# Optimization experiments

Measured on AMD Instinct MI355X. Metric: run time of the kernel, lower is better.

The kernel has to match this reference:

```python
import jax, jax.numpy as jnp
import numpy as np

B, S, D, H, DK, DV = 4, 1024, 1024, 16, 64, 64
NEG = jnp.float32(-1e10)


def setup_inputs() -> dict:
    key = jax.random.key(0)
    ks = jax.random.split(key, 9)
    q = jax.random.normal(ks[0], (B, S, D), dtype=jnp.float32)
    k = jax.random.normal(ks[1], (B, S, D), dtype=jnp.float32)
    v = jax.random.normal(ks[2], (B, S, D), dtype=jnp.float32)
    pad_mask_1 = jax.random.randint(ks[3], (B,), 1, S + 1, dtype=jnp.int32)
    pad_mask_2 = jax.random.randint(ks[4], (B,), 1, S + 1, dtype=jnp.int32)
    # Per-head projection weights stacked over heads (torch Linear, bias=False).
    sc = 1.0 / np.sqrt(D)
    Wq = jax.random.uniform(ks[5], (H, D, DK), jnp.float32, -sc, sc)
    Wk = jax.random.uniform(ks[6], (H, D, DK), jnp.float32, -sc, sc)
    Wv = jax.random.uniform(ks[7], (H, D, DV), jnp.float32, -sc, sc)
    Wo = jax.random.uniform(ks[8], (H * DV, D), jnp.float32, -sc, sc)
    return {"q": q, "k": k, "v": v, "pad_mask_1": pad_mask_1,
            "pad_mask_2": pad_mask_2, "Wq": Wq, "Wk": Wk, "Wv": Wv, "Wo": Wo}


def reference(q, k, v, pad_mask_1, pad_mask_2, Wq, Wk, Wv, Wo):
    Bq, Sq, _ = q.shape
    scale = jnp.sqrt(jnp.float32(Wq.shape[-1]))
    qh = jnp.einsum('bsd,hdk->bhsk', q, Wq)   # [B,H,S,DK]
    kh = jnp.einsum('bsd,hdk->bhsk', k, Wk)
    vh = jnp.einsum('bsd,hdv->bhsv', v, Wv)
    w = jnp.einsum('bhqk,bhtk->bhqt', qh, kh) / scale  # [B,H,S,S]
    idx = jnp.arange(Sq)
    # pad_mask_1: mask key columns >= length; pad_mask_2: mask query rows >= length
    key_dead = idx[None, :] >= pad_mask_1[:, None]      # [B,S]
    row_dead = idx[None, :] >= pad_mask_2[:, None]      # [B,S]
    w = jnp.where(key_dead[:, None, None, :], NEG, w)
    w = jnp.where(row_dead[:, None, :, None], NEG, w)
    # causal: w.tril() + (-1e10).triu(1) == keep lower triangle, NEG strictly above
    causal = idx[None, :] > idx[:, None]                # [S,S] strictly upper
    w = jnp.where(causal[None, None], NEG, w)
    a = jax.nn.softmax(w, axis=-1)
    o = jnp.einsum('bhqt,bhtv->bhqv', a, vh)            # [B,H,S,DV]
    o = o.transpose(0, 2, 1, 3).reshape(Bq, Sq, -1)     # concat heads (head-major)
    return o @ Wo
```

## Files before the change

kernel.cpp:

```cpp
#include <hip/hip_runtime.h>

#define B_ 4
#define S_ 1024
#define D_ 1024
#define H_ 16
#define BSD (B_*S_*D_)

typedef unsigned short ushort_t;
typedef __attribute__((ext_vector_type(8))) __bf16 bf16x8;
typedef __attribute__((ext_vector_type(4))) float f32x4;

__device__ __forceinline__ ushort_t f2bf(float f) {
  union { float f; unsigned int u; } x; x.f = f;
  unsigned int r = x.u + 0x7fffu + ((x.u >> 16) & 1u);
  return (ushort_t)(r >> 16);
}

__device__ __forceinline__ void gll16(const void* g, void* l) {
  __builtin_amdgcn_global_load_lds(
      (const __attribute__((address_space(1))) unsigned int*)g,
      (__attribute__((address_space(3))) unsigned int*)l, 16, 0, 0);
}

__global__ __launch_bounds__(256) void convert_qkv(
    const float* __restrict__ q, const float* __restrict__ k, const float* __restrict__ v,
    ushort_t* __restrict__ qb, ushort_t* __restrict__ kb, ushort_t* __restrict__ vb)
{
  int z = blockIdx.y;
  const float* src = (z == 0) ? q : (z == 1) ? k : v;
  ushort_t* dst = (z == 0) ? qb : (z == 1) ? kb : vb;
  int idx = (blockIdx.x * 256 + threadIdx.x) * 4;
  float4 f = *(const float4*)(src + idx);
  ushort4 r;
  r.x = f2bf(f.x); r.y = f2bf(f.y); r.z = f2bf(f.z); r.w = f2bf(f.w);
  *(ushort4*)(dst + idx) = r;
}

__global__ __launch_bounds__(256) void transpose_w(
    const float* __restrict__ Wq, const float* __restrict__ Wk,
    const float* __restrict__ Wv, const float* __restrict__ Wo,
    ushort_t* __restrict__ WqT, ushort_t* __restrict__ WkT,
    ushort_t* __restrict__ WvT, ushort_t* __restrict__ WoT)
{
  __shared__ float tile[64][65];
  int blk = blockIdx.x;
  const float* src; ushort_t* dst;
  size_t sbase, dbase; int ld_src, ld_dst, r0, c0;
  if (blk < 768) {
    int tz = blk / 256;
    int rem = blk % 256; int head = rem >> 4; int kt = rem & 15;
    src = (tz == 0) ? Wq : (tz == 1) ? Wk : Wv;
    dst = (tz == 0) ? WqT : (tz == 1) ? WkT : WvT;
    sbase = (size_t)head * 1024 * 64; dbase = (size_t)head * 64 * 1024;
    ld_src = 64; ld_dst = 1024; r0 = kt * 64; c0 = 0;
  } else {
    int idx = blk - 768; src = Wo; dst = WoT;
    sbase = 0; dbase = 0; ld_src = 1024; ld_dst = 1024;
    r0 = (idx >> 4) * 64; c0 = (idx & 15) * 64;
  }
  int tid = threadIdx.x; int col = tid & 63; int rbase = tid >> 6;
  #pragma unroll
  for (int j = 0; j < 16; ++j) {
    int row = j * 4 + rbase;
    tile[row][col] = src[sbase + (size_t)(r0 + row) * ld_src + c0 + col];
  }
  __syncthreads();
  #pragma unroll
  for (int j = 0; j < 16; ++j) {
    int orow = j * 4 + rbase;
    dst[dbase + (size_t)(c0 + orow) * ld_dst + r0 + col] = f2bf(tile[col][orow]);
  }
}

__device__ __forceinline__ void gemm_body(
    const ushort_t* __restrict__ A, const ushort_t* __restrict__ BT,
    ushort_t* __restrict__ Cb, float* __restrict__ Cf,
    int epi, int m0, int n0, int K)
{
  __shared__ __align__(16) ushort_t As[2][128 * 64];
  __shared__ __align__(16) ushort_t Bs[2][128 * 64];
  const int tid = threadIdx.x;
  const int wave = tid >> 6, lane = tid & 63;
  const int wm = wave >> 2, wn = wave & 3;

  f32x4 acc[4][2] = {};

  auto stage = [&](int buf, int k0) {
    #pragma unroll
    for (int i = 0; i < 2; ++i) {
      int off = ((i * 8 + wave) << 10) + lane * 16;
      int row = off >> 7;
      int cb = off & 127;
      int lcb = cb ^ ((row & 7) << 4);
      gll16(A + (size_t)(m0 + row) * K + k0 + (lcb >> 1), (char*)As[buf] + off);
      gll16(BT + (size_t)(n0 + row) * K + k0 + (lcb >> 1), (char*)Bs[buf] + off);
    }
  };

  auto compute = [&](int buf) {
    #pragma unroll
    for (int kk = 0; kk < 2; ++kk) {
      bf16x8 af[4], bfr[2];
      #pragma unroll
      for (int mf = 0; mf < 4; ++mf) {
        int row = wm * 64 + mf * 16 + (lane & 15);
        int cb = kk * 64 + ((lane >> 4) << 4);
        af[mf] = *(const bf16x8*)((const char*)As[buf] + (row << 7) + (cb ^ ((row & 7) << 4)));
      }
      #pragma unroll
      for (int nf = 0; nf < 2; ++nf) {
        int row = wn * 32 + nf * 16 + (lane & 15);
        int cb = kk * 64 + ((lane >> 4) << 4);
        bfr[nf] = *(const bf16x8*)((const char*)Bs[buf] + (row << 7) + (cb ^ ((row & 7) << 4)));
      }
      #pragma unroll
      for (int mf = 0; mf < 4; ++mf)
        #pragma unroll
        for (int nf = 0; nf < 2; ++nf)
          acc[mf][nf] = __builtin_amdgcn_mfma_f32_16x16x32_bf16(af[mf], bfr[nf], acc[mf][nf], 0, 0, 0);
    }
  };

  const int nt = K >> 6;
  stage(0, 0);
  __syncthreads();
  int cur = 0;
  for (int t = 0; t < nt - 1; ++t) {
    stage(cur ^ 1, (t + 1) << 6);
    compute(cur);
    __syncthreads();
    cur ^= 1;
  }
  compute(cur);

  #pragma unroll
  for (int mf = 0; mf < 4; ++mf) {
    #pragma unroll
    for (int nf = 0; nf < 2; ++nf) {
      #pragma unroll
      for (int r = 0; r < 4; ++r) {
        int m = m0 + wm * 64 + mf * 16 + ((lane >> 4) << 2) + r;
        int n = n0 + wn * 32 + nf * 16 + (lane & 15);
        float val = acc[mf][nf][r];
        if (epi == 0) {
          int b = m >> 10, s = m & 1023, h = n >> 6, dk = n & 63;
          Cb[((((size_t)(b * H_ + h)) << 10) + s) * 64 + dk] = f2bf(val);
        } else if (epi == 1) {
          int b = m >> 10, s = m & 1023, h = n >> 6, dv = n & 63;
          Cb[((((size_t)(b * H_ + h)) * 64 + dv) << 10) + s] = f2bf(val);
        } else {
          Cf[(size_t)m * 1024 + n] = val;
        }
      }
    }
  }
}

__global__ __launch_bounds__(512, 4) void proj_gemm(
    const ushort_t* qb, const ushort_t* kb, const ushort_t* vb,
    const ushort_t* WqT, const ushort_t* WkT, const ushort_t* WvT,
    ushort_t* qh, ushort_t* kh, ushort_t* vhT)
{
  int f = blockIdx.x;
  int xcd = f & 7;
  int slot = f >> 3;
  int g = xcd * 12 + (slot >> 3);
  int y = slot & 7;
  int z = g >> 5, x = g & 31;
  const ushort_t* A = (z == 0) ? qb : (z == 1) ? kb : vb;
  const ushort_t* BT = (z == 0) ? WqT : (z == 1) ? WkT : WvT;
  ushort_t* C = (z == 0) ? qh : (z == 1) ? kh : vhT;
  gemm_body(A, BT, C, nullptr, (z == 2) ? 1 : 0, x * 128, y * 128, 1024);
}

__global__ __launch_bounds__(512, 4) void out_gemm(
    const ushort_t* o, const ushort_t* WoT, float* out)
{
  int f = blockIdx.x;
  int xcd = f & 7;
  int slot = f >> 3;
  int x = xcd * 4 + (slot >> 3);
  int y = slot & 7;
  gemm_body(o, WoT, nullptr, out, 2, x * 128, y * 128, 1024);
}

__global__ __launch_bounds__(256) void meanv_kernel(
    const ushort_t* __restrict__ vhT, float* __restrict__ meanV)
{
  int row = blockIdx.x * 4 + (threadIdx.x >> 6);
  int lane = threadIdx.x & 63;
  const ushort_t* src = vhT + ((size_t)row << 10) + lane * 16;
  float s = 0.f;
  #pragma unroll
  for (int i = 0; i < 2; ++i) {
    bf16x8 v = *(const bf16x8*)(src + i * 8);
    #pragma unroll
    for (int j = 0; j < 8; ++j) s += (float)v[j];
  }
  #pragma unroll
  for (int mm = 1; mm < 64; mm <<= 1) s += __shfl_xor(s, mm);
  if (lane == 0) meanV[row] = s * (1.0f / 1024.0f);
}

__global__ __launch_bounds__(256) void attn_kernel(
    const ushort_t* __restrict__ qh, const ushort_t* __restrict__ kh,
    const ushort_t* __restrict__ vhT, const float* __restrict__ meanV,
    const int* __restrict__ pad1p, const int* __restrict__ pad2p,
    ushort_t* __restrict__ o)
{
  const int bh = blockIdx.x;
  const int b = bh >> 4, h = bh & 15;
  const int q0 = blockIdx.y << 6;
  const int pad1 = pad1p[b], pad2 = pad2p[b];
  const int tid = threadIdx.x, wave = tid >> 6, lane = tid & 63;

  if (q0 >= pad2) {
    int dv = tid & 63;
    int rw = tid >> 6;
    ushort_t mb = f2bf(meanV[(bh << 6) + dv]);
    for (int r = rw; r < 64; r += 4)
      o[(((size_t)((b << 10) + q0 + r)) << 10) + (h << 6) + dv] = mb;
    return;
  }

  __shared__ __align__(16) ushort_t Ks[64 * 64];
  __shared__ __align__(16) ushort_t Vs[64 * 64];
  __shared__ __align__(16) ushort_t Ps[4][16 * 64];

  const ushort_t* qbase = qh + ((size_t)bh << 16);
  const ushort_t* kbase = kh + ((size_t)bh << 16);
  const ushort_t* vbase = vhT + ((size_t)bh << 16);

  const int qrow = q0 + wave * 16 + (lane & 15);
  bf16x8 qf[2];
  qf[0] = *(const bf16x8*)(qbase + (size_t)qrow * 64 + ((lane >> 4) << 3));
  qf[1] = *(const bf16x8*)(qbase + (size_t)qrow * 64 + 32 + ((lane >> 4) << 3));

  f32x4 acc[4] = {};
  float mrow[4] = { -1e30f, -1e30f, -1e30f, -1e30f };
  float lrow[4] = { 0.f, 0.f, 0.f, 0.f };
  const int ribase = q0 + wave * 16 + ((lane >> 4) << 2);

  int t_hi = min(q0 + 63, min(pad2 - 1, pad1 - 1));
  int nb = (t_hi >> 6) + 1;

  for (int kb = 0; kb < nb; ++kb) {
    const int t0 = kb << 6;
    #pragma unroll
    for (int i = 0; i < 2; ++i) {
      int off = ((i * 4 + wave) << 10) + lane * 16;
      int row = off >> 7;
      int cb = off & 127;
      int lcb = cb ^ ((row & 7) << 4);
      gll16(kbase + (size_t)(t0 + row) * 64 + (lcb >> 1), (char*)Ks + off);
      gll16(vbase + ((size_t)row << 10) + t0 + (lcb >> 1), (char*)Vs + off);
    }
    __syncthreads();

    f32x4 sc[4];
    #pragma unroll
    for (int nf = 0; nf < 4; ++nf) {
      sc[nf] = (f32x4){0.f, 0.f, 0.f, 0.f};
      #pragma unroll
      for (int kk = 0; kk < 2; ++kk) {
        int trow = nf * 16 + (lane & 15);
        int cb = kk * 64 + ((lane >> 4) << 4);
        bf16x8 kf = *(const bf16x8*)((const char*)Ks + (trow << 7) + (cb ^ ((trow & 7) << 4)));
        sc[nf] = __builtin_amdgcn_mfma_f32_16x16x32_bf16(qf[kk], kf, sc[nf], 0, 0, 0);
      }
    }

    float pv[4][4];
    #pragma unroll
    for (int r = 0; r < 4; ++r) {
      const int irow = ribase + r;
      float sval[4];
      float rmax = -1e30f;
      #pragma unroll
      for (int nf = 0; nf < 4; ++nf) {
        int t = t0 + nf * 16 + (lane & 15);
        float vv = sc[nf][r] * 0.125f;
        if (t > irow || t >= pad1) vv = -1e10f;
        sval[nf] = vv;
        rmax = fmaxf(rmax, vv);
      }
      #pragma unroll
      for (int mm = 1; mm < 16; mm <<= 1) rmax = fmaxf(rmax, __shfl_xor(rmax, mm));
      float nm = fmaxf(mrow[r], rmax);
      float fscale = __expf(mrow[r] - nm);
      float rsum = 0.f;
      #pragma unroll
      for (int nf = 0; nf < 4; ++nf) {
        float p = __expf(sval[nf] - nm);
        pv[nf][r] = p;
        rsum += p;
      }
      #pragma unroll
      for (int mm = 1; mm < 16; mm <<= 1) rsum += __shfl_xor(rsum, mm);
      mrow[r] = nm;
      lrow[r] = lrow[r] * fscale + rsum;
      #pragma unroll
      for (int dvf = 0; dvf < 4; ++dvf) acc[dvf][r] *= fscale;
    }

    #pragma unroll
    for (int nf = 0; nf < 4; ++nf) {
      #pragma unroll
      for (int r = 0; r < 4; ++r) {
        int prow = ((lane >> 4) << 2) + r;
        int cbw = (nf * 16 + (lane & 15)) * 2;
        *(ushort_t*)((char*)Ps[wave] + (prow << 7) + (cbw ^ ((prow & 7) << 4))) = f2bf(pv[nf][r]);
      }
    }

    #pragma unroll
    for (int kk = 0; kk < 2; ++kk) {
      int prow = lane & 15;
      int cb = kk * 64 + ((lane >> 4) << 4);
      bf16x8 pf = *(const bf16x8*)((const char*)Ps[wave] + (prow << 7) + (cb ^ ((prow & 7) << 4)));
      #pragma unroll
      for (int dvf = 0; dvf < 4; ++dvf) {
        int vrow = dvf * 16 + (lane & 15);
        bf16x8 vfr = *(const bf16x8*)((const char*)Vs + (vrow << 7) + (cb ^ ((vrow & 7) << 4)));
        acc[dvf] = __builtin_amdgcn_mfma_f32_16x16x32_bf16(pf, vfr, acc[dvf], 0, 0, 0);
      }
    }
    __syncthreads();
  }

  #pragma unroll
  for (int dvf = 0; dvf < 4; ++dvf) {
    #pragma unroll
    for (int r = 0; r < 4; ++r) {
      int irow = ribase + r;
      int dv = dvf * 16 + (lane & 15);
      float val;
      if (irow < pad2) val = acc[dvf][r] * (1.0f / lrow[r]);
      else val = meanV[(bh << 6) + dv];
      o[(((size_t)((b << 10) + irow)) << 10) + (h << 6) + dv] = f2bf(val);
    }
  }
}

extern "C" void kernel_launch(void* const* d_in, const int* in_sizes, int n_in,
                              void* d_out, int out_size, void* d_ws, size_t ws_size,
                              hipStream_t stream) {
  (void)in_sizes; (void)n_in; (void)out_size; (void)ws_size;
  const float* q = (const float*)d_in[0];
  const float* k = (const float*)d_in[1];
  const float* v = (const float*)d_in[2];
  const int* pad1 = (const int*)d_in[3];
  const int* pad2 = (const int*)d_in[4];
  const float* Wq = (const float*)d_in[5];
  const float* Wk = (const float*)d_in[6];
  const float* Wv = (const float*)d_in[7];
  const float* Wo = (const float*)d_in[8];
  float* out = (float*)d_out;

  char* ws = (char*)d_ws;
  const size_t MB = 1u << 20;
  ushort_t* qb  = (ushort_t*)(ws + 0 * MB);
  ushort_t* kb  = (ushort_t*)(ws + 8 * MB);
  ushort_t* vb  = (ushort_t*)(ws + 16 * MB);
  ushort_t* WqT = (ushort_t*)(ws + 24 * MB);
  ushort_t* WkT = (ushort_t*)(ws + 26 * MB);
  ushort_t* WvT = (ushort_t*)(ws + 28 * MB);
  ushort_t* WoT = (ushort_t*)(ws + 30 * MB);
  ushort_t* qh  = (ushort_t*)(ws + 32 * MB);
  ushort_t* kh  = (ushort_t*)(ws + 40 * MB);
  ushort_t* vhT = (ushort_t*)(ws + 48 * MB);
  ushort_t* ob  = (ushort_t*)(ws + 56 * MB);
  float* meanV  = (float*)(ws + 64 * MB);

  convert_qkv<<<dim3(BSD / 1024, 3), 256, 0, stream>>>(q, k, v, qb, kb, vb);
  transpose_w<<<1024, 256, 0, stream>>>(Wq, Wk, Wv, Wo, WqT, WkT, WvT, WoT);
  proj_gemm<<<768, 512, 0, stream>>>(qb, kb, vb, WqT, WkT, WvT, qh, kh, vhT);
  meanv_kernel<<<1024, 256, 0, stream>>>(vhT, meanV);
  attn_kernel<<<dim3(64, 16), 256, 0, stream>>>(qh, kh, vhT, meanV, pad1, pad2, ob);
  out_gemm<<<256, 512, 0, stream>>>(ob, WoT, out);
}
```

Baseline: 113.4 us.

## Use 256x256 tiles with a ping-pong staged pipeline for QKV projection GEMM

```diff
diff --git a/kernel.cpp b/kernel.cpp
--- a/kernel.cpp
+++ b/kernel.cpp
@@ -156,21 +156,169 @@
   }
 }
 
-__global__ __launch_bounds__(512, 4) void proj_gemm(
+__device__ __forceinline__ void gemm256_body(
+    const ushort_t* __restrict__ A, const ushort_t* __restrict__ BT,
+    ushort_t* __restrict__ Cb, int epi, int m0, int n0, int K)
+{
+  __shared__ __align__(16) ushort_t As[2][256 * 64];
+  __shared__ __align__(16) ushort_t Bs[2][256 * 64];
+  const int tid = threadIdx.x;
+  const int wave = tid >> 6, lane = tid & 63;
+  const int wm = wave >> 2, wn = wave & 3;
+
+  f32x4 acc[8][4] = {};
+  bf16x8 af[4][2];
+  bf16x8 bfr[2][2];
+
+#define STAGE_A(BUF, HALF, K0) do { \
+    _Pragma("unroll") \
+    for (int i_ = 0; i_ < 2; ++i_) { \
+      int off_ = ((i_ * 8 + wave) << 10) + lane * 16; \
+      int row_ = off_ >> 7, cb_ = off_ & 127; \
+      int lcb_ = cb_ ^ ((row_ & 7) << 4); \
+      gll16(A + (size_t)(m0 + (HALF) * 128 + row_) * K + (K0) + (lcb_ >> 1), \
+            (char*)As[BUF] + (HALF) * 16384 + off_); \
+    } } while (0)
+
+#define STAGE_B(BUF, HALF, K0) do { \
+    _Pragma("unroll") \
+    for (int i_ = 0; i_ < 2; ++i_) { \
+      int off_ = ((i_ * 8 + wave) << 10) + lane * 16; \
+      int row_ = off_ >> 7, cb_ = off_ & 127; \
+      int lcb_ = cb_ ^ ((row_ & 7) << 4); \
+      gll16(BT + (size_t)(n0 + (HALF) * 128 + row_) * K + (K0) + (lcb_ >> 1), \
+            (char*)Bs[BUF] + (HALF) * 16384 + off_); \
+    } } while (0)
+
+#define LOAD_A(BUF, MH) do { \
+    _Pragma("unroll") \
+    for (int kk_ = 0; kk_ < 2; ++kk_) \
+      _Pragma("unroll") \
+      for (int mf_ = 0; mf_ < 4; ++mf_) { \
+        int row_ = wm * 128 + (MH) * 64 + mf_ * 16 + (lane & 15); \
+        int cb_ = kk_ * 64 + ((lane >> 4) << 4); \
+        af[mf_][kk_] = *(const bf16x8*)((const char*)As[BUF] + (row_ << 7) + (cb_ ^ ((row_ & 7) << 4))); \
+      } } while (0)
+
+#define LOAD_B(BUF, NH) do { \
+    _Pragma("unroll") \
+    for (int kk_ = 0; kk_ < 2; ++kk_) \
+      _Pragma("unroll") \
+      for (int nf_ = 0; nf_ < 2; ++nf_) { \
+        int row_ = wn * 64 + (NH) * 32 + nf_ * 16 + (lane & 15); \
+        int cb_ = kk_ * 64 + ((lane >> 4) << 4); \
+        bfr[nf_][kk_] = *(const bf16x8*)((const char*)Bs[BUF] + (row_ << 7) + (cb_ ^ ((row_ & 7) << 4))); \
+      } } while (0)
+
+#define MMA_Q(MH, NH) do { \
+    __builtin_amdgcn_s_setprio(1); \
+    _Pragma("unroll") \
+    for (int kk_ = 0; kk_ < 2; ++kk_) \
+      _Pragma("unroll") \
+      for (int mf_ = 0; mf_ < 4; ++mf_) \
+        _Pragma("unroll") \
+        for (int nf_ = 0; nf_ < 2; ++nf_) \
+          acc[(MH) * 4 + mf_][(NH) * 2 + nf_] = __builtin_amdgcn_mfma_f32_16x16x32_bf16( \
+              af[mf_][kk_], bfr[nf_][kk_], acc[(MH) * 4 + mf_][(NH) * 2 + nf_], 0, 0, 0); \
+    __builtin_amdgcn_s_setprio(0); \
+  } while (0)
+
+#define BAR()   __builtin_amdgcn_s_barrier()
+#define LGKM0() asm volatile("s_waitcnt lgkmcnt(0)" ::: "memory")
+#define VM(N)   asm volatile("s_waitcnt vmcnt(" #N ")" ::: "memory")
+
+  STAGE_A(0, 0, 0);
+  STAGE_B(0, 0, 0);
+  STAGE_B(0, 1, 0);
+  STAGE_A(0, 1, 0);
+  STAGE_A(1, 0, 64);
+  VM(6);
+  BAR();
+
+  const int NT = K >> 6;
+  for (int t = 0; t < NT - 2; t += 2) {
+    const int k1 = (t + 1) << 6, k2 = (t + 2) << 6, k3 = (t + 3) << 6;
+    LOAD_A(0, 0); LOAD_B(0, 0); STAGE_B(1, 0, k1);
+    BAR(); LGKM0(); MMA_Q(0, 0); VM(6); BAR();
+    LOAD_B(0, 1);               STAGE_B(1, 1, k1);
+    BAR(); LGKM0(); MMA_Q(0, 1); VM(6); BAR();
+    LOAD_A(0, 1); LOAD_B(0, 0); STAGE_A(1, 1, k1);
+    BAR(); LGKM0(); MMA_Q(1, 0); VM(6); BAR();
+    LOAD_B(0, 1);               STAGE_A(0, 0, k2);
+    BAR(); LGKM0(); MMA_Q(1, 1); VM(6); BAR();
+    LOAD_A(1, 0); LOAD_B(1, 0); STAGE_B(0, 0, k2);
+    BAR(); LGKM0(); MMA_Q(0, 0); VM(6); BAR();
+    LOAD_B(1, 1);               STAGE_B(0, 1, k2);
+    BAR(); LGKM0(); MMA_Q(0, 1); VM(6); BAR();
+    LOAD_A(1, 1); LOAD_B(1, 0); STAGE_A(0, 1, k2);
+    BAR(); LGKM0(); MMA_Q(1, 0); VM(6); BAR();
+    LOAD_B(1, 1);               STAGE_A(1, 0, k3);
+    BAR(); LGKM0(); MMA_Q(1, 1); VM(6); BAR();
+  }
+  {
+    const int k1 = (NT - 1) << 6;
+    LOAD_A(0, 0); LOAD_B(0, 0); STAGE_B(1, 0, k1);
+    BAR(); LGKM0(); MMA_Q(0, 0); VM(6); BAR();
+    LOAD_B(0, 1);               STAGE_B(1, 1, k1);
+    BAR(); LGKM0(); MMA_Q(0, 1); VM(6); BAR();
+    LOAD_A(0, 1); LOAD_B(0, 0); STAGE_A(1, 1, k1);
+    BAR(); LGKM0(); MMA_Q(1, 0); VM(6); BAR();
+    LOAD_B(0, 1);
+    BAR(); LGKM0(); MMA_Q(1, 1); VM(4); BAR();
+    LOAD_A(1, 0); LOAD_B(1, 0);
+    BAR(); LGKM0(); MMA_Q(0, 0); VM(2); BAR();
+    LOAD_B(1, 1);
+    BAR(); LGKM0(); MMA_Q(0, 1); VM(0); BAR();
+    LOAD_A(1, 1); LOAD_B(1, 0);
+    BAR(); LGKM0(); MMA_Q(1, 0); BAR();
+    LOAD_B(1, 1);
+    LGKM0(); MMA_Q(1, 1);
+  }
+
+#undef STAGE_A
+#undef STAGE_B
+#undef LOAD_A
+#undef LOAD_B
+#undef MMA_Q
+#undef BAR
+#undef LGKM0
+#undef VM
+
+  #pragma unroll
+  for (int mi = 0; mi < 8; ++mi) {
+    #pragma unroll
+    for (int ni = 0; ni < 4; ++ni) {
+      #pragma unroll
+      for (int r = 0; r < 4; ++r) {
+        int m = m0 + wm * 128 + (mi >> 2) * 64 + (mi & 3) * 16 + ((lane >> 4) << 2) + r;
+        int n = n0 + wn * 64 + (ni >> 1) * 32 + (ni & 1) * 16 + (lane & 15);
+        float val = acc[mi][ni][r];
+        if (epi == 0) {
+          int b = m >> 10, s = m & 1023, h = n >> 6, dk = n & 63;
+          Cb[((((size_t)(b * H_ + h)) << 10) + s) * 64 + dk] = f2bf(val);
+        } else {
+          int b = m >> 10, s = m & 1023, h = n >> 6, dv = n & 63;
+          Cb[((((size_t)(b * H_ + h)) * 64 + dv) << 10) + s] = f2bf(val);
+        }
+      }
+    }
+  }
+}
+
+__global__ __launch_bounds__(512, 2) void proj_gemm256(
     const ushort_t* qb, const ushort_t* kb, const ushort_t* vb,
     const ushort_t* WqT, const ushort_t* WkT, const ushort_t* WvT,
     ushort_t* qh, ushort_t* kh, ushort_t* vhT)
 {
   int f = blockIdx.x;
-  int xcd = f & 7;
-  int slot = f >> 3;
-  int g = xcd * 12 + (slot >> 3);
-  int y = slot & 7;
-  int z = g >> 5, x = g & 31;
+  int g = (f & 7) * 24 + (f >> 3);
+  int z = g >> 6;
+  int rem = g & 63;
+  int x = rem >> 2, y = rem & 3;
   const ushort_t* A = (z == 0) ? qb : (z == 1) ? kb : vb;
   const ushort_t* BT = (z == 0) ? WqT : (z == 1) ? WkT : WvT;
   ushort_t* C = (z == 0) ? qh : (z == 1) ? kh : vhT;
-  gemm_body(A, BT, C, nullptr, (z == 2) ? 1 : 0, x * 128, y * 128, 1024);
+  gemm256_body(A, BT, C, (z == 2) ? 1 : 0, x * 256, y * 256, 1024);
 }
 
 __global__ __launch_bounds__(512, 4) void out_gemm(
@@ -374,7 +522,7 @@
 
   convert_qkv<<<dim3(BSD / 1024, 3), 256, 0, stream>>>(q, k, v, qb, kb, vb);
   transpose_w<<<1024, 256, 0, stream>>>(Wq, Wk, Wv, Wo, WqT, WkT, WvT, WoT);
-  proj_gemm<<<768, 512, 0, stream>>>(qb, kb, vb, WqT, WkT, WvT, qh, kh, vhT);
+  proj_gemm256<<<192, 512, 0, stream>>>(qb, kb, vb, WqT, WkT, WvT, qh, kh, vhT);
   meanv_kernel<<<1024, 256, 0, stream>>>(vhT, meanV);
   attn_kernel<<<dim3(64, 16), 256, 0, stream>>>(qh, kh, vhT, meanV, pad1, pad2, ob);
   out_gemm<<<256, 512, 0, stream>>>(ob, WoT, out);
```

After: 124.3 us. 1.1x slower.

## Fuse fp32-to-bf16 conversion of q/k/v into projection GEMM A-tile loads

Applied to the files above, without the earlier changes.

```diff
diff --git a/kernel.cpp b/kernel.cpp
--- a/kernel.cpp
+++ b/kernel.cpp
@@ -8,6 +8,7 @@
 
 typedef unsigned short ushort_t;
 typedef __attribute__((ext_vector_type(8))) __bf16 bf16x8;
+typedef __attribute__((ext_vector_type(8))) ushort_t ushortx8;
 typedef __attribute__((ext_vector_type(4))) float f32x4;
 
 __device__ __forceinline__ ushort_t f2bf(float f) {
@@ -20,20 +21,6 @@
   __builtin_amdgcn_global_load_lds(
       (const __attribute__((address_space(1))) unsigned int*)g,
       (__attribute__((address_space(3))) unsigned int*)l, 16, 0, 0);
-}
-
-__global__ __launch_bounds__(256) void convert_qkv(
-    const float* __restrict__ q, const float* __restrict__ k, const float* __restrict__ v,
-    ushort_t* __restrict__ qb, ushort_t* __restrict__ kb, ushort_t* __restrict__ vb)
-{
-  int z = blockIdx.y;
-  const float* src = (z == 0) ? q : (z == 1) ? k : v;
-  ushort_t* dst = (z == 0) ? qb : (z == 1) ? kb : vb;
-  int idx = (blockIdx.x * 256 + threadIdx.x) * 4;
-  float4 f = *(const float4*)(src + idx);
-  ushort4 r;
-  r.x = f2bf(f.x); r.y = f2bf(f.y); r.z = f2bf(f.z); r.w = f2bf(f.w);
-  *(ushort4*)(dst + idx) = r;
 }
 
 __global__ __launch_bounds__(256) void transpose_w(
@@ -72,10 +59,119 @@
   }
 }
 
+__device__ __forceinline__ void gemm_body_f32A(
+    const float* __restrict__ Af, const ushort_t* __restrict__ BT,
+    ushort_t* __restrict__ Cb, int epi, int m0, int n0, int K)
+{
+  __shared__ __align__(16) ushort_t As[2][128 * 64];
+  __shared__ __align__(16) ushort_t Bs[2][128 * 64];
+  const int tid = threadIdx.x;
+  const int wave = tid >> 6, lane = tid & 63;
+  const int wm = wave >> 2, wn = wave & 3;
+
+  f32x4 acc[4][2] = {};
+  float4 areg[2][2];
+
+  auto loadA = [&](int k0) {
+    #pragma unroll
+    for (int i = 0; i < 2; ++i) {
+      int off = ((i * 8 + wave) << 10) + lane * 16;
+      int row = off >> 7;
+      int cb = off & 127;
+      int lcb = cb ^ ((row & 7) << 4);
+      const float* src = Af + (size_t)(m0 + row) * K + k0 + (lcb >> 1);
+      areg[i][0] = *(const float4*)(src);
+      areg[i][1] = *(const float4*)(src + 4);
+    }
+  };
+  auto writeA = [&](int buf) {
+    #pragma unroll
+    for (int i = 0; i < 2; ++i) {
+      int off = ((i * 8 + wave) << 10) + lane * 16;
+      ushortx8 t;
+      #pragma unroll
+      for (int j = 0; j < 4; ++j) {
+        t[j]     = f2bf(((const float*)&areg[i][0])[j]);
+        t[4 + j] = f2bf(((const float*)&areg[i][1])[j]);
+      }
+      *(ushortx8*)((char*)As[buf] + off) = t;
+    }
+  };
+  auto stageB = [&](int buf, int k0) {
+    #pragma unroll
+    for (int i = 0; i < 2; ++i) {
+      int off = ((i * 8 + wave) << 10) + lane * 16;
+      int row = off >> 7;
+      int cb = off & 127;
+      int lcb = cb ^ ((row & 7) << 4);
+      gll16(BT + (size_t)(n0 + row) * K + k0 + (lcb >> 1), (char*)Bs[buf] + off);
+    }
+  };
+
+  auto compute = [&](int buf) {
+    #pragma unroll
+    for (int kk = 0; kk < 2; ++kk) {
+      bf16x8 af[4], bfr[2];
+      #pragma unroll
+      for (int mf = 0; mf < 4; ++mf) {
+        int row = wm * 64 + mf * 16 + (lane & 15);
+        int cb = kk * 64 + ((lane >> 4) << 4);
+        af[mf] = *(const bf16x8*)((const char*)As[buf] + (row << 7) + (cb ^ ((row & 7) << 4)));
+      }
+      #pragma unroll
+      for (int nf = 0; nf < 2; ++nf) {
+        int row = wn * 32 + nf * 16 + (lane & 15);
+        int cb = kk * 64 + ((lane >> 4) << 4);
+        bfr[nf] = *(const bf16x8*)((const char*)Bs[buf] + (row << 7) + (cb ^ ((row & 7) << 4)));
+      }
+      #pragma unroll
+      for (int mf = 0; mf < 4; ++mf)
+        #pragma unroll
+        for (int nf = 0; nf < 2; ++nf)
+          acc[mf][nf] = __builtin_amdgcn_mfma_f32_16x16x32_bf16(af[mf], bfr[nf], acc[mf][nf], 0, 0, 0);
+    }
+  };
+
+  const int nt = K >> 6;
+  loadA(0);
+  stageB(0, 0);
+  writeA(0);
+  __syncthreads();
+  int cur = 0;
+  for (int t = 0; t < nt - 1; ++t) {
+    loadA((t + 1) << 6);
+    stageB(cur ^ 1, (t + 1) << 6);
+    compute(cur);
+    writeA(cur ^ 1);
+    __syncthreads();
+    cur ^= 1;
+  }
+  compute(cur);
+
+  #pragma unroll
+  for (int mf = 0; mf < 4; ++mf) {
+    #pragma unroll
+    for (int nf = 0; nf < 2; ++nf) {
+      #pragma unroll
+      for (int r = 0; r < 4; ++r) {
+        int m = m0 + wm * 64 + mf * 16 + ((lane >> 4) << 2) + r;
+        int n = n0 + wn * 32 + nf * 16 + (lane & 15);
+        float val = acc[mf][nf][r];
+        if (epi == 0) {
+          int b = m >> 10, s = m & 1023, h = n >> 6, dk = n & 63;
+          Cb[((((size_t)(b * H_ + h)) << 10) + s) * 64 + dk] = f2bf(val);
+        } else {
+          int b = m >> 10, s = m & 1023, h = n >> 6, dv = n & 63;
+          Cb[((((size_t)(b * H_ + h)) * 64 + dv) << 10) + s] = f2bf(val);
+        }
+      }
+    }
+  }
+}
+
 __device__ __forceinline__ void gemm_body(
     const ushort_t* __restrict__ A, const ushort_t* __restrict__ BT,
-    ushort_t* __restrict__ Cb, float* __restrict__ Cf,
-    int epi, int m0, int n0, int K)
+    float* __restrict__ Cf, int m0, int n0, int K)
 {
   __shared__ __align__(16) ushort_t As[2][128 * 64];
   __shared__ __align__(16) ushort_t Bs[2][128 * 64];
@@ -141,23 +237,14 @@
       for (int r = 0; r < 4; ++r) {
         int m = m0 + wm * 64 + mf * 16 + ((lane >> 4) << 2) + r;
         int n = n0 + wn * 32 + nf * 16 + (lane & 15);
-        float val = acc[mf][nf][r];
-        if (epi == 0) {
-          int b = m >> 10, s = m & 1023, h = n >> 6, dk = n & 63;
-          Cb[((((size_t)(b * H_ + h)) << 10) + s) * 64 + dk] = f2bf(val);
-        } else if (epi == 1) {
-          int b = m >> 10, s = m & 1023, h = n >> 6, dv = n & 63;
-          Cb[((((size_t)(b * H_ + h)) * 64 + dv) << 10) + s] = f2bf(val);
-        } else {
-          Cf[(size_t)m * 1024 + n] = val;
-        }
+        Cf[(size_t)m * 1024 + n] = acc[mf][nf][r];
       }
     }
   }
 }
 
 __global__ __launch_bounds__(512, 4) void proj_gemm(
-    const ushort_t* qb, const ushort_t* kb, const ushort_t* vb,
+    const float* q, const float* k, const float* v,
     const ushort_t* WqT, const ushort_t* WkT, const ushort_t* WvT,
     ushort_t* qh, ushort_t* kh, ushort_t* vhT)
 {
@@ -167,10 +254,10 @@
   int g = xcd * 12 + (slot >> 3);
   int y = slot & 7;
   int z = g >> 5, x = g & 31;
-  const ushort_t* A = (z == 0) ? qb : (z == 1) ? kb : vb;
+  const float* A = (z == 0) ? q : (z == 1) ? k : v;
   const ushort_t* BT = (z == 0) ? WqT : (z == 1) ? WkT : WvT;
   ushort_t* C = (z == 0) ? qh : (z == 1) ? kh : vhT;
-  gemm_body(A, BT, C, nullptr, (z == 2) ? 1 : 0, x * 128, y * 128, 1024);
+  gemm_body_f32A(A, BT, C, (z == 2) ? 1 : 0, x * 128, y * 128, 1024);
 }
 
 __global__ __launch_bounds__(512, 4) void out_gemm(
@@ -181,7 +268,7 @@
   int slot = f >> 3;
   int x = xcd * 4 + (slot >> 3);
   int y = slot & 7;
-  gemm_body(o, WoT, nullptr, out, 2, x * 128, y * 128, 1024);
+  gemm_body(o, WoT, out, x * 128, y * 128, 1024);
 }
 
 __global__ __launch_bounds__(256) void meanv_kernel(
@@ -359,9 +446,6 @@
 
   char* ws = (char*)d_ws;
   const size_t MB = 1u << 20;
-  ushort_t* qb  = (ushort_t*)(ws + 0 * MB);
-  ushort_t* kb  = (ushort_t*)(ws + 8 * MB);
-  ushort_t* vb  = (ushort_t*)(ws + 16 * MB);
   ushort_t* WqT = (ushort_t*)(ws + 24 * MB);
   ushort_t* WkT = (ushort_t*)(ws + 26 * MB);
   ushort_t* WvT = (ushort_t*)(ws + 28 * MB);
@@ -372,9 +456,8 @@
   ushort_t* ob  = (ushort_t*)(ws + 56 * MB);
   float* meanV  = (float*)(ws + 64 * MB);
 
-  convert_qkv<<<dim3(BSD / 1024, 3), 256, 0, stream>>>(q, k, v, qb, kb, vb);
   transpose_w<<<1024, 256, 0, stream>>>(Wq, Wk, Wv, Wo, WqT, WkT, WvT, WoT);
-  proj_gemm<<<768, 512, 0, stream>>>(qb, kb, vb, WqT, WkT, WvT, qh, kh, vhT);
+  proj_gemm<<<768, 512, 0, stream>>>(q, k, v, WqT, WkT, WvT, qh, kh, vhT);
   meanv_kernel<<<1024, 256, 0, stream>>>(vhT, meanV);
   attn_kernel<<<dim3(64, 16), 256, 0, stream>>>(qh, kh, vhT, meanV, pad1, pad2, ob);
   out_gemm<<<256, 512, 0, stream>>>(ob, WoT, out);
```

Result: no change. 112.2 us (-1.0%).
